# Optimization experiments

Hardware: AMD Instinct MI355X
Metric: run time of the kernel (lower is better)

## Reference

```python
import jax, jax.numpy as jnp
import numpy as np

TOP_K = 2
EPS = 1e-6


def setup_inputs() -> dict:
    key = jax.random.key(0)
    ks = jax.random.split(key, 4)
    T, H, D, E = 8192, 2048, 2048, 8
    std = 0.02
    return {
        "x": jax.random.normal(ks[0], (T, H), dtype=jnp.float32),
        "router_scale": jnp.ones((H,), dtype=jnp.float32),
        "per_expert_scale": jnp.ones((E,), dtype=jnp.float32),
        "router_w": jax.random.normal(ks[1], (E, H), dtype=jnp.float32) * std,
        "gate_up_proj": jax.random.normal(ks[2], (E, 2 * D, H), dtype=jnp.float32) * std,
        "down_proj": jax.random.normal(ks[3], (E, H, D), dtype=jnp.float32) * std,
    }


def reference(x, router_scale, per_expert_scale, router_w, gate_up_proj, down_proj):
    T, H = x.shape
    E = router_w.shape[0]
    D = down_proj.shape[-1]

    # RMSNorm (no learned scale) + router scaling
    r = x * jax.lax.rsqrt(jnp.mean(x * x, axis=-1, keepdims=True) + EPS)
    r = r * router_scale * (H ** -0.5)

    logits = (r @ router_w.T).astype(jnp.float32)          # [T, E]
    probs = jax.nn.softmax(logits, axis=-1)
    _, topk_idx = jax.lax.top_k(logits, TOP_K)             # [T, k]
    w = jnp.take_along_axis(probs, topk_idx, axis=-1)      # [T, k]
    w = w / jnp.sum(w, axis=-1, keepdims=True)
    w = w * per_expert_scale[topk_idx]

    # Dense combine weights [T, E]; zero for non-selected experts (topk indices
    # are distinct per token, so .set is collision-free).
    combine = jnp.zeros((T, E), dtype=x.dtype)
    combine = combine.at[jnp.arange(T)[:, None], topk_idx].set(w.astype(x.dtype))

    out = jnp.zeros_like(x)
    for e in range(E):  # fixed small loop over experts (structural, not data dim)
        gu = x @ gate_up_proj[e].T                          # [T, 2D]
        gate, up = gu[:, :D], gu[:, D:]
        h = jax.nn.gelu(gate, approximate=True) * up        # GLU with tanh-gelu
        out = out + combine[:, e:e + 1] * (h @ down_proj[e].T)
    return out
```

## Files before the change

kernel.cpp:

```cpp
#include <hip/hip_runtime.h>
#include <hip/hip_bf16.h>
#include <math.h>

#define TT 8192
#define HH 2048
#define DD 2048
#define EE 8
#define NT 32

typedef short bf16x8 __attribute__((ext_vector_type(8)));
typedef float f32x4 __attribute__((ext_vector_type(4)));

__device__ __forceinline__ ushort f2bf(float f){
  unsigned u = __float_as_uint(f);
  u += 0x7fffu + ((u>>16)&1u);
  return (ushort)(u>>16);
}

#define GLOAD16(SRC,DST) \
  __builtin_amdgcn_global_load_lds((const __attribute__((address_space(1))) void*)(SRC), \
                                   (__attribute__((address_space(3))) void*)(DST), 16, 0, 0)

#define SBAR __builtin_amdgcn_sched_barrier(0)
#define BARR __builtin_amdgcn_s_barrier()
#define WLG  asm volatile("s_waitcnt lgkmcnt(0)" ::: "memory")
#define WVM6 asm volatile("s_waitcnt vmcnt(6)" ::: "memory")
#define PRI(x) __builtin_amdgcn_s_setprio(x)

__global__ __launch_bounds__(256) void cvt_kernel(const float* __restrict__ src,
                                                  ushort* __restrict__ dst, size_t n){
  size_t i = ((size_t)blockIdx.x*256 + threadIdx.x)*8;
  size_t stride = (size_t)gridDim.x*256*8;
  for (; i < n; i += stride){
    float4 a = *(const float4*)(src+i);
    float4 b = *(const float4*)(src+i+4);
    uint4 v;
    v.x = (unsigned)f2bf(a.x) | ((unsigned)f2bf(a.y)<<16);
    v.y = (unsigned)f2bf(a.z) | ((unsigned)f2bf(a.w)<<16);
    v.z = (unsigned)f2bf(b.x) | ((unsigned)f2bf(b.y)<<16);
    v.w = (unsigned)f2bf(b.z) | ((unsigned)f2bf(b.w)<<16);
    *(uint4*)(dst+i) = v;
  }
}

__global__ __launch_bounds__(256) void router_kernel(
    const float* __restrict__ x, const float* __restrict__ rscale,
    const float* __restrict__ pes, const float* __restrict__ rw,
    ushort* __restrict__ x16, int* __restrict__ cnt,
    int* __restrict__ tok, float* __restrict__ wgt, int4* __restrict__ tmap)
{
  int t = blockIdx.x;
  int tid = threadIdx.x;
  const float4* xr  = (const float4*)(x + (size_t)t*HH);
  const float4* rs4 = (const float4*)rscale;
  float4 xa = xr[tid], xb = xr[tid+256];
  float4 sa = rs4[tid], sb = rs4[tid+256];
  double xd[8] = {xa.x,xa.y,xa.z,xa.w,xb.x,xb.y,xb.z,xb.w};
  double sd[8] = {sa.x,sa.y,sa.z,sa.w,sb.x,sb.y,sb.z,sb.w};
  double acc[9];
  double ss = 0.0;
  #pragma unroll
  for (int j=0;j<8;j++) ss += xd[j]*xd[j];
  acc[8] = ss;
  double xs[8];
  #pragma unroll
  for (int j=0;j<8;j++) xs[j] = xd[j]*sd[j];
  #pragma unroll
  for (int e=0;e<EE;e++){
    const float4* w4 = (const float4*)(rw + (size_t)e*HH);
    float4 wa = w4[tid], wb = w4[tid+256];
    double wd[8] = {wa.x,wa.y,wa.z,wa.w,wb.x,wb.y,wb.z,wb.w};
    double d = 0.0;
    #pragma unroll
    for (int j=0;j<8;j++) d += xs[j]*wd[j];
    acc[e] = d;
  }
  uint2 pa, pb;
  pa.x = (unsigned)f2bf(xa.x) | ((unsigned)f2bf(xa.y)<<16);
  pa.y = (unsigned)f2bf(xa.z) | ((unsigned)f2bf(xa.w)<<16);
  pb.x = (unsigned)f2bf(xb.x) | ((unsigned)f2bf(xb.y)<<16);
  pb.y = (unsigned)f2bf(xb.z) | ((unsigned)f2bf(xb.w)<<16);
  uint2* xo = (uint2*)(x16 + (size_t)t*HH);
  xo[tid] = pa; xo[tid+256] = pb;

  __shared__ double red[9*256];
  #pragma unroll
  for (int j=0;j<9;j++) red[j*256+tid] = acc[j];
  __syncthreads();
  for (int s=128;s>0;s>>=1){
    if (tid < s){
      #pragma unroll
      for (int j=0;j<9;j++) red[j*256+tid] += red[j*256+tid+s];
    }
    __syncthreads();
  }
  if (tid==0){
    double mean = red[8*256] / (double)HH;
    double rms  = 1.0 / sqrt(mean + 1e-6);
    double sc   = rms / sqrt((double)HH);
    double l[EE];
    #pragma unroll
    for (int e=0;e<EE;e++) l[e] = red[e*256]*sc;
    int i0 = 0;
    #pragma unroll
    for (int e=1;e<EE;e++) if (l[e] > l[i0]) i0 = e;
    int i1 = -1;
    #pragma unroll
    for (int e=0;e<EE;e++){ if (e==i0) continue; if (i1 < 0 || l[e] > l[i1]) i1 = e; }
    double p1 = exp(l[i1]-l[i0]);
    double s  = 1.0 + p1;
    float w0 = (float)((1.0/s) * (double)pes[i0]);
    float w1 = (float)((p1 /s) * (double)pes[i1]);
    int pos0 = atomicAdd(&cnt[i0],1);
    tok[i0*TT+pos0] = t; wgt[i0*TT+pos0] = w0;
    int pos1 = atomicAdd(&cnt[i1],1);
    tok[i1*TT+pos1] = t; wgt[i1*TT+pos1] = w1;
    tmap[t] = make_int4(i0,pos0,i1,pos1);
  }
}

__global__ void scan_kernel(const int* __restrict__ cnt, int* __restrict__ off){
  if (threadIdx.x==0 && blockIdx.x==0){
    int a = 0;
    for (int e=0;e<EE;e++){ off[e]=a; a+=cnt[e]; }
    off[EE]=a;
  }
}

#define STA(bb,h,t) do{ \
    GLOAD16(pA[2*(h)  ] + (size_t)(t)*64, &ldsA[bb][(h)*8192        + wid*512]); \
    GLOAD16(pA[2*(h)+1] + (size_t)(t)*64, &ldsA[bb][(h)*8192 + 4096 + wid*512]); }while(0)
#define STB(bb,h,t) do{ \
    GLOAD16(pB[2*(h)  ] + (size_t)(t)*64, &ldsB[bb][(h)*8192        + wid*512]); \
    GLOAD16(pB[2*(h)+1] + (size_t)(t)*64, &ldsB[bb][(h)*8192 + 4096 + wid*512]); }while(0)

#define RD_A(h) do{ _Pragma("unroll") \
  for (int mf=0;mf<4;mf++){ int row=(h)*128 + wm*64 + mf*16 + frow; \
    a[mf][0] = *(const bf16x8*)&As[row*64 + c0]; \
    a[mf][1] = *(const bf16x8*)&As[row*64 + c1]; } }while(0)
#define RD_B(h,bb_) do{ _Pragma("unroll") \
  for (int nf=0;nf<2;nf++){ int row=(h)*128 + wn*32 + nf*16 + frow; \
    bb_[nf][0] = *(const bf16x8*)&Bs[row*64 + c0]; \
    bb_[nf][1] = *(const bf16x8*)&Bs[row*64 + c1]; } }while(0)

#define MMQ(mo,no,bb_) do{ _Pragma("unroll") \
  for (int mf=0;mf<4;mf++){ _Pragma("unroll") \
    for (int nf=0;nf<2;nf++){ \
      acc[(mo)+mf][(no)+nf] = __builtin_amdgcn_mfma_f32_16x16x32_bf16(a[mf][0], bb_[nf][0], acc[(mo)+mf][(no)+nf],0,0,0); \
      acc[(mo)+mf][(no)+nf] = __builtin_amdgcn_mfma_f32_16x16x32_bf16(a[mf][1], bb_[nf][1], acc[(mo)+mf][(no)+nf],0,0,0); } } }while(0)

#define KLOOP for (int t=0;t<NT;t++){ \
    int cur=t&1, nxt=cur^1; \
    const ushort* As=&ldsA[cur][0]; const ushort* Bs=&ldsB[cur][0]; \
    RD_A(0); RD_B(0,b0); \
    if (t+1<NT) STA(nxt,1,t+1); \
    SBAR; BARR; WLG; SBAR; PRI(1); MMQ(0,0,b0); PRI(0); SBAR; BARR; SBAR; \
    RD_B(1,b1); \
    if (t+2<NT) STA(cur,0,t+2); \
    SBAR; BARR; WLG; SBAR; PRI(1); MMQ(0,2,b1); PRI(0); SBAR; BARR; SBAR; \
    RD_A(1); \
    if (t+2<NT) STB(cur,0,t+2); \
    SBAR; BARR; WLG; SBAR; PRI(1); MMQ(4,0,b0); PRI(0); SBAR; BARR; SBAR; \
    if (t+2<NT) STB(cur,1,t+2); \
    SBAR; BARR; SBAR; PRI(1); MMQ(4,2,b1); PRI(0); SBAR; WVM6; BARR; SBAR; \
  }

#define PROLOGUE \
  STA(0,0,0); STB(0,0,0); STB(0,1,0); STA(0,1,0); \
  STA(1,0,1); STB(1,0,1); STB(1,1,1); \
  SBAR; WVM6; BARR; SBAR;

__global__ __launch_bounds__(512,2) void ffn1_kernel(
    const ushort* __restrict__ x16, const ushort* __restrict__ w13,
    const int* __restrict__ cnt, const int* __restrict__ off,
    const int* __restrict__ tok, ushort* __restrict__ hbuf)
{
  int f = blockIdx.x + 16*(blockIdx.y + 32*blockIdx.z);
  int w = ((f&7)<<9) + (f>>3);
  int e  = w >> 9;
  int n0 = (w & 15) << 7;
  int m0 = ((w >> 4) & 31) << 8;
  int ce = cnt[e];
  if (m0 >= ce) return;

  __shared__ ushort ldsA[2][256*64];
  __shared__ ushort ldsB[2][256*64];

  int tid = threadIdx.x, wid = tid>>6, lane = tid&63;
  int wm = wid>>2, wn = wid&3;
  int frow = lane&15, klane = lane>>4;
  int c0 = ((klane  ) ^ (frow&7))<<3;
  int c1 = ((klane+4) ^ (frow&7))<<3;

  int r   = wid*8 + (lane>>3);
  int csw = ((lane&7) ^ (lane>>3))<<3;

  const ushort* pA[4]; const ushort* pB[4];
  int oe = off[e];
  #pragma unroll
  for (int k=0;k<4;k++){
    int R  = k*64 + r;
    int ar = min(m0+R, ce-1);
    pA[k] = x16 + (size_t)tok[e*TT+ar]*HH + csw;
    int p = 2*k + (r>>5), mat = (r>>4)&1;
    pB[k] = w13 + (size_t)e*(2*DD)*HH + (size_t)(mat*DD + n0 + p*16 + (r&15))*HH + csw;
  }

  f32x4 acc[8][4];
  #pragma unroll
  for (int i=0;i<8;i++)
    #pragma unroll
    for (int j=0;j<4;j++) acc[i][j] = {0.f,0.f,0.f,0.f};
  bf16x8 a[4][2], b0[2][2], b1[2][2];

  PROLOGUE
  KLOOP

  #pragma unroll
  for (int mf=0;mf<8;mf++){
    int rb = ((mf<4)? wm*64 + mf*16 : 128 + wm*64 + (mf-4)*16) + klane*4;
    #pragma unroll
    for (int q=0;q<4;q++){
      int gm = m0 + rb + q;
      if (gm < ce){
        size_t hrow = (size_t)(oe+gm)*DD;
        #pragma unroll
        for (int pp=0;pp<2;pp++){
          float g = acc[mf][2*pp][q], u = acc[mf][2*pp+1][q];
          float t2 = 1.5957691216057308f*(g + 0.044715f*g*g*g);
          float sg = 1.f/(1.f+__expf(-t2));
          hbuf[hrow + n0 + pp*64 + wn*16 + frow] = f2bf(g*u*sg);
        }
      }
    }
  }
}

__global__ __launch_bounds__(512,2) void ffn2_kernel(
    const ushort* __restrict__ hbuf, const ushort* __restrict__ w2,
    const int* __restrict__ cnt, const int* __restrict__ off,
    ushort* __restrict__ ybuf)
{
  int f = blockIdx.x + 8*(blockIdx.y + 32*blockIdx.z);
  int w = ((f&7)<<8) + (f>>3);
  int e  = w >> 8;
  int n0 = (w & 7) << 8;
  int m0 = ((w >> 3) & 31) << 8;
  int ce = cnt[e];
  if (m0 >= ce) return;

  __shared__ ushort ldsA[2][256*64];
  __shared__ ushort ldsB[2][256*64];

  int tid = threadIdx.x, wid = tid>>6, lane = tid&63;
  int wm = wid>>2, wn = wid&3;
  int frow = lane&15, klane = lane>>4;
  int c0 = ((klane  ) ^ (frow&7))<<3;
  int c1 = ((klane+4) ^ (frow&7))<<3;

  int r   = wid*8 + (lane>>3);
  int csw = ((lane&7) ^ (lane>>3))<<3;

  const ushort* pA[4]; const ushort* pB[4];
  int oe = off[e];
  #pragma unroll
  for (int k=0;k<4;k++){
    int R  = k*64 + r;
    int ar = oe + min(m0+R, ce-1);
    pA[k] = hbuf + (size_t)ar*DD + csw;
    pB[k] = w2 + (size_t)e*HH*DD + (size_t)(n0 + R)*DD + csw;
  }

  f32x4 acc[8][4];
  #pragma unroll
  for (int i=0;i<8;i++)
    #pragma unroll
    for (int j=0;j<4;j++) acc[i][j] = {0.f,0.f,0.f,0.f};
  bf16x8 a[4][2], b0[2][2], b1[2][2];

  PROLOGUE
  KLOOP

  #pragma unroll
  for (int mf=0;mf<8;mf++){
    int rb = ((mf<4)? wm*64 + mf*16 : 128 + wm*64 + (mf-4)*16) + klane*4;
    #pragma unroll
    for (int q=0;q<4;q++){
      int gm = m0 + rb + q;
      if (gm < ce){
        size_t yrow = (size_t)(oe+gm)*HH;
        #pragma unroll
        for (int nf=0;nf<4;nf++){
          int col = (nf>>1)*128 + wn*32 + (nf&1)*16 + frow;
          ybuf[yrow + n0 + col] = f2bf(acc[mf][nf][q]);
        }
      }
    }
  }
}

__global__ __launch_bounds__(256) void combine_kernel(
    const ushort* __restrict__ ybuf, const int4* __restrict__ tmap,
    const float* __restrict__ wgt, const int* __restrict__ off,
    float* __restrict__ out)
{
  int t = blockIdx.x, tid = threadIdx.x;
  int4 m = tmap[t];
  float w0 = wgt[m.x*TT + m.y];
  float w1 = wgt[m.z*TT + m.w];
  const ushort* y0 = ybuf + (size_t)(off[m.x] + m.y)*HH + tid*8;
  const ushort* y1 = ybuf + (size_t)(off[m.z] + m.w)*HH + tid*8;
  uint4 v0 = *(const uint4*)y0;
  uint4 v1 = *(const uint4*)y1;
  float* o = out + (size_t)t*HH + tid*8;
  const unsigned* a0 = (const unsigned*)&v0;
  const unsigned* a1 = (const unsigned*)&v1;
  float r[8];
  #pragma unroll
  for (int j=0;j<4;j++){
    float lo0 = __uint_as_float(a0[j]<<16), hi0 = __uint_as_float(a0[j]&0xffff0000u);
    float lo1 = __uint_as_float(a1[j]<<16), hi1 = __uint_as_float(a1[j]&0xffff0000u);
    r[2*j]   = w0*lo0 + w1*lo1;
    r[2*j+1] = w0*hi0 + w1*hi1;
  }
  *(float4*)o     = make_float4(r[0],r[1],r[2],r[3]);
  *(float4*)(o+4) = make_float4(r[4],r[5],r[6],r[7]);
}

extern "C" void kernel_launch(void* const* d_in, const int* in_sizes, int n_in,
                              void* d_out, int out_size, void* d_ws, size_t ws_size,
                              hipStream_t stream)
{
  const float* x    = (const float*)d_in[0];
  const float* rsc  = (const float*)d_in[1];
  const float* pes  = (const float*)d_in[2];
  const float* rw   = (const float*)d_in[3];
  const float* w13f = (const float*)d_in[4];
  const float* w2f  = (const float*)d_in[5];
  float* out = (float*)d_out;

  char* ws = (char*)d_ws;
  size_t o_x16 = 0;
  size_t o_w13 = o_x16 + (size_t)TT*HH*2;
  size_t o_w2  = o_w13 + (size_t)EE*2*DD*HH*2;
  size_t o_h   = o_w2  + (size_t)EE*HH*DD*2;
  size_t o_cnt = o_h   + (size_t)2*TT*DD*2;
  size_t o_off = o_cnt + 128;
  size_t o_tok = o_off + 128;
  size_t o_wgt = o_tok + (size_t)EE*TT*4;
  size_t o_map = o_wgt + (size_t)EE*TT*4;
  size_t need  = o_map + (size_t)TT*16;

  if (ws_size < need){ hipMemsetAsync(d_out, 0, (size_t)TT*HH*4, stream); return; }

  ushort* x16 = (ushort*)(ws + o_x16);
  ushort* w13 = (ushort*)(ws + o_w13);
  ushort* w2  = (ushort*)(ws + o_w2);
  ushort* hbuf= (ushort*)(ws + o_h);
  ushort* ybuf= (ushort*)(ws + o_w13);
  int*   cnt  = (int*)(ws + o_cnt);
  int*   off  = (int*)(ws + o_off);
  int*   tok  = (int*)(ws + o_tok);
  float* wgt  = (float*)(ws + o_wgt);
  int4*  tmap = (int4*)(ws + o_map);

  hipMemsetAsync(cnt, 0, EE*sizeof(int), stream);
  cvt_kernel<<<4096,256,0,stream>>>(w13f, w13, (size_t)EE*2*DD*HH);
  cvt_kernel<<<2048,256,0,stream>>>(w2f,  w2,  (size_t)EE*HH*DD);
  router_kernel<<<TT,256,0,stream>>>(x, rsc, pes, rw, x16, cnt, tok, wgt, tmap);
  scan_kernel<<<1,64,0,stream>>>(cnt, off);
  dim3 g1(DD/128, TT/256, EE);
  ffn1_kernel<<<g1,512,0,stream>>>(x16, w13, cnt, off, tok, hbuf);
  dim3 g2(HH/256, TT/256, EE);
  ffn2_kernel<<<g2,512,0,stream>>>(hbuf, w2, cnt, off, ybuf);
  combine_kernel<<<TT,256,0,stream>>>(ybuf, tmap, wgt, off, out);
}
```

Measured before the change: 791.3 us.

## Fuse fp32-to-bf16 weight conversion into expert GEMM B-tile loads

Removes the separate weight conversion kernels and has both FFN GEMMs load fp32 weights into registers, convert them to bf16 and store them into swizzled LDS. The k-loop pipeline is reordered so the register load for step t+2 and the LDS write for step t+1 overlap with MFMA work. This removes a full pass over all expert weights. In exchange, the weights are read in fp32 by every active m-tile, and register pressure rises.

```diff
diff --git a/kernel.cpp b/kernel.cpp
--- a/kernel.cpp
+++ b/kernel.cpp
@@ -24,24 +24,7 @@
 #define SBAR __builtin_amdgcn_sched_barrier(0)
 #define BARR __builtin_amdgcn_s_barrier()
 #define WLG  asm volatile("s_waitcnt lgkmcnt(0)" ::: "memory")
-#define WVM6 asm volatile("s_waitcnt vmcnt(6)" ::: "memory")
 #define PRI(x) __builtin_amdgcn_s_setprio(x)
-
-__global__ __launch_bounds__(256) void cvt_kernel(const float* __restrict__ src,
-                                                  ushort* __restrict__ dst, size_t n){
-  size_t i = ((size_t)blockIdx.x*256 + threadIdx.x)*8;
-  size_t stride = (size_t)gridDim.x*256*8;
-  for (; i < n; i += stride){
-    float4 a = *(const float4*)(src+i);
-    float4 b = *(const float4*)(src+i+4);
-    uint4 v;
-    v.x = (unsigned)f2bf(a.x) | ((unsigned)f2bf(a.y)<<16);
-    v.y = (unsigned)f2bf(a.z) | ((unsigned)f2bf(a.w)<<16);
-    v.z = (unsigned)f2bf(b.x) | ((unsigned)f2bf(b.y)<<16);
-    v.w = (unsigned)f2bf(b.z) | ((unsigned)f2bf(b.w)<<16);
-    *(uint4*)(dst+i) = v;
-  }
-}
 
 __global__ __launch_bounds__(256) void router_kernel(
     const float* __restrict__ x, const float* __restrict__ rscale,
@@ -130,9 +113,17 @@
 #define STA(bb,h,t) do{ \
     GLOAD16(pA[2*(h)  ] + (size_t)(t)*64, &ldsA[bb][(h)*8192        + wid*512]); \
     GLOAD16(pA[2*(h)+1] + (size_t)(t)*64, &ldsA[bb][(h)*8192 + 4096 + wid*512]); }while(0)
-#define STB(bb,h,t) do{ \
-    GLOAD16(pB[2*(h)  ] + (size_t)(t)*64, &ldsB[bb][(h)*8192        + wid*512]); \
-    GLOAD16(pB[2*(h)+1] + (size_t)(t)*64, &ldsB[bb][(h)*8192 + 4096 + wid*512]); }while(0)
+
+#define BLOAD(t) do{ _Pragma("unroll") \
+  for (int j=0;j<8;j++) breg[j] = *(const float4*)(pBsrc + (size_t)(t)*64 + j*4); }while(0)
+#define BWRITE(bb) do{ _Pragma("unroll") \
+  for (int j=0;j<4;j++){ \
+    uint4 v; \
+    v.x=(unsigned)f2bf(breg[2*j  ].x)|((unsigned)f2bf(breg[2*j  ].y)<<16); \
+    v.y=(unsigned)f2bf(breg[2*j  ].z)|((unsigned)f2bf(breg[2*j  ].w)<<16); \
+    v.z=(unsigned)f2bf(breg[2*j+1].x)|((unsigned)f2bf(breg[2*j+1].y)<<16); \
+    v.w=(unsigned)f2bf(breg[2*j+1].z)|((unsigned)f2bf(breg[2*j+1].w)<<16); \
+    *(uint4*)&ldsB[bb][(bwr<<6) + (((bch*4+j) ^ (bwr&7))<<3)] = v; } }while(0)
 
 #define RD_A(h) do{ _Pragma("unroll") \
   for (int mf=0;mf<4;mf++){ int row=(h)*128 + wm*64 + mf*16 + frow; \
@@ -153,25 +144,27 @@
     int cur=t&1, nxt=cur^1; \
     const ushort* As=&ldsA[cur][0]; const ushort* Bs=&ldsB[cur][0]; \
     RD_A(0); RD_B(0,b0); \
-    if (t+1<NT) STA(nxt,1,t+1); \
     SBAR; BARR; WLG; SBAR; PRI(1); MMQ(0,0,b0); PRI(0); SBAR; BARR; SBAR; \
     RD_B(1,b1); \
     if (t+2<NT) STA(cur,0,t+2); \
     SBAR; BARR; WLG; SBAR; PRI(1); MMQ(0,2,b1); PRI(0); SBAR; BARR; SBAR; \
     RD_A(1); \
-    if (t+2<NT) STB(cur,0,t+2); \
+    if (t+1<NT) BWRITE(nxt); \
     SBAR; BARR; WLG; SBAR; PRI(1); MMQ(4,0,b0); PRI(0); SBAR; BARR; SBAR; \
-    if (t+2<NT) STB(cur,1,t+2); \
-    SBAR; BARR; SBAR; PRI(1); MMQ(4,2,b1); PRI(0); SBAR; WVM6; BARR; SBAR; \
+    if (t+2<NT){ STA(cur,1,t+2); BLOAD(t+2); } \
+    SBAR; BARR; SBAR; PRI(1); MMQ(4,2,b1); PRI(0); SBAR; BARR; SBAR; \
   }
 
 #define PROLOGUE \
-  STA(0,0,0); STB(0,0,0); STB(0,1,0); STA(0,1,0); \
-  STA(1,0,1); STB(1,0,1); STB(1,1,1); \
-  SBAR; WVM6; BARR; SBAR;
+  BLOAD(0); \
+  STA(0,0,0); STA(0,1,0); STA(1,0,1); STA(1,1,1); \
+  BWRITE(0); \
+  BLOAD(1); \
+  asm volatile("s_waitcnt vmcnt(12)" ::: "memory"); \
+  WLG; BARR; SBAR;
 
 __global__ __launch_bounds__(512,2) void ffn1_kernel(
-    const ushort* __restrict__ x16, const ushort* __restrict__ w13,
+    const ushort* __restrict__ x16, const float* __restrict__ w13,
     const int* __restrict__ cnt, const int* __restrict__ off,
     const int* __restrict__ tok, ushort* __restrict__ hbuf)
 {
@@ -195,16 +188,18 @@
   int r   = wid*8 + (lane>>3);
   int csw = ((lane&7) ^ (lane>>3))<<3;
 
-  const ushort* pA[4]; const ushort* pB[4];
+  const ushort* pA[4];
   int oe = off[e];
   #pragma unroll
   for (int k=0;k<4;k++){
     int R  = k*64 + r;
     int ar = min(m0+R, ce-1);
     pA[k] = x16 + (size_t)tok[e*TT+ar]*HH + csw;
-    int p = 2*k + (r>>5), mat = (r>>4)&1;
-    pB[k] = w13 + (size_t)e*(2*DD)*HH + (size_t)(mat*DD + n0 + p*16 + (r&15))*HH + csw;
-  }
+  }
+  int bwr = tid & 255, bch = tid >> 8;
+  const float* pBsrc = w13 + (size_t)e*(2*DD)*HH
+                     + (size_t)(((bwr>>4)&1)*DD + n0 + (bwr>>5)*16 + (bwr&15))*HH
+                     + bch*32;
 
   f32x4 acc[8][4];
   #pragma unroll
@@ -212,6 +207,7 @@
     #pragma unroll
     for (int j=0;j<4;j++) acc[i][j] = {0.f,0.f,0.f,0.f};
   bf16x8 a[4][2], b0[2][2], b1[2][2];
+  float4 breg[8];
 
   PROLOGUE
   KLOOP
@@ -237,7 +233,7 @@
 }
 
 __global__ __launch_bounds__(512,2) void ffn2_kernel(
-    const ushort* __restrict__ hbuf, const ushort* __restrict__ w2,
+    const ushort* __restrict__ hbuf, const float* __restrict__ w2,
     const int* __restrict__ cnt, const int* __restrict__ off,
     ushort* __restrict__ ybuf)
 {
@@ -261,15 +257,16 @@
   int r   = wid*8 + (lane>>3);
   int csw = ((lane&7) ^ (lane>>3))<<3;
 
-  const ushort* pA[4]; const ushort* pB[4];
+  const ushort* pA[4];
   int oe = off[e];
   #pragma unroll
   for (int k=0;k<4;k++){
     int R  = k*64 + r;
     int ar = oe + min(m0+R, ce-1);
     pA[k] = hbuf + (size_t)ar*DD + csw;
-    pB[k] = w2 + (size_t)e*HH*DD + (size_t)(n0 + R)*DD + csw;
-  }
+  }
+  int bwr = tid & 255, bch = tid >> 8;
+  const float* pBsrc = w2 + (size_t)e*HH*DD + (size_t)(n0 + bwr)*DD + bch*32;
 
   f32x4 acc[8][4];
   #pragma unroll
@@ -277,6 +274,7 @@
     #pragma unroll
     for (int j=0;j<4;j++) acc[i][j] = {0.f,0.f,0.f,0.f};
   bf16x8 a[4][2], b0[2][2], b1[2][2];
+  float4 breg[8];
 
   PROLOGUE
   KLOOP
@@ -341,10 +339,9 @@
 
   char* ws = (char*)d_ws;
   size_t o_x16 = 0;
-  size_t o_w13 = o_x16 + (size_t)TT*HH*2;
-  size_t o_w2  = o_w13 + (size_t)EE*2*DD*HH*2;
-  size_t o_h   = o_w2  + (size_t)EE*HH*DD*2;
-  size_t o_cnt = o_h   + (size_t)2*TT*DD*2;
+  size_t o_h   = o_x16 + (size_t)TT*HH*2;
+  size_t o_y   = o_h   + (size_t)2*TT*DD*2;
+  size_t o_cnt = o_y   + (size_t)2*TT*HH*2;
   size_t o_off = o_cnt + 128;
   size_t o_tok = o_off + 128;
   size_t o_wgt = o_tok + (size_t)EE*TT*4;
@@ -354,10 +351,8 @@
   if (ws_size < need){ hipMemsetAsync(d_out, 0, (size_t)TT*HH*4, stream); return; }
 
   ushort* x16 = (ushort*)(ws + o_x16);
-  ushort* w13 = (ushort*)(ws + o_w13);
-  ushort* w2  = (ushort*)(ws + o_w2);
   ushort* hbuf= (ushort*)(ws + o_h);
-  ushort* ybuf= (ushort*)(ws + o_w13);
+  ushort* ybuf= (ushort*)(ws + o_y);
   int*   cnt  = (int*)(ws + o_cnt);
   int*   off  = (int*)(ws + o_off);
   int*   tok  = (int*)(ws + o_tok);
@@ -365,13 +360,11 @@
   int4*  tmap = (int4*)(ws + o_map);
 
   hipMemsetAsync(cnt, 0, EE*sizeof(int), stream);
-  cvt_kernel<<<4096,256,0,stream>>>(w13f, w13, (size_t)EE*2*DD*HH);
-  cvt_kernel<<<2048,256,0,stream>>>(w2f,  w2,  (size_t)EE*HH*DD);
   router_kernel<<<TT,256,0,stream>>>(x, rsc, pes, rw, x16, cnt, tok, wgt, tmap);
   scan_kernel<<<1,64,0,stream>>>(cnt, off);
   dim3 g1(DD/128, TT/256, EE);
-  ffn1_kernel<<<g1,512,0,stream>>>(x16, w13, cnt, off, tok, hbuf);
+  ffn1_kernel<<<g1,512,0,stream>>>(x16, w13f, cnt, off, tok, hbuf);
   dim3 g2(HH/256, TT/256, EE);
-  ffn2_kernel<<<g2,512,0,stream>>>(hbuf, w2, cnt, off, ybuf);
+  ffn2_kernel<<<g2,512,0,stream>>>(hbuf, w2f, cnt, off, ybuf);
   combine_kernel<<<TT,256,0,stream>>>(ybuf, tmap, wgt, off, out);
 }
```

Result: slower. 1.377 ms (+74.0%).

## Fuse weight bf16 conversions into router and ffn1 kernels

Applied to the files above, without the earlier changes.

Removes the two standalone fp32-to-bf16 conversion kernels. The gate_up weight conversion now runs as a grid-stride tail of the router kernel, and the down_proj conversion runs as a tail of the ffn1 kernel, including in blocks that have no tokens and previously exited early. This saves two launches and lets the bandwidth-bound conversion overlap with router and GEMM work. In exchange it adds memory traffic inside the ffn1 GEMM, which may slow it, and it relies on the ffn1 grid size being hard-coded to 4096 blocks.

```diff
diff --git a/kernel.cpp b/kernel.cpp
--- a/kernel.cpp
+++ b/kernel.cpp
@@ -27,27 +27,22 @@
 #define WVM6 asm volatile("s_waitcnt vmcnt(6)" ::: "memory")
 #define PRI(x) __builtin_amdgcn_s_setprio(x)
 
-__global__ __launch_bounds__(256) void cvt_kernel(const float* __restrict__ src,
-                                                  ushort* __restrict__ dst, size_t n){
-  size_t i = ((size_t)blockIdx.x*256 + threadIdx.x)*8;
-  size_t stride = (size_t)gridDim.x*256*8;
-  for (; i < n; i += stride){
-    float4 a = *(const float4*)(src+i);
-    float4 b = *(const float4*)(src+i+4);
-    uint4 v;
-    v.x = (unsigned)f2bf(a.x) | ((unsigned)f2bf(a.y)<<16);
-    v.y = (unsigned)f2bf(a.z) | ((unsigned)f2bf(a.w)<<16);
-    v.z = (unsigned)f2bf(b.x) | ((unsigned)f2bf(b.y)<<16);
-    v.w = (unsigned)f2bf(b.z) | ((unsigned)f2bf(b.w)<<16);
-    *(uint4*)(dst+i) = v;
-  }
-}
+#define CVT8(SRCP,DSTP,CI) do{ \
+    const float* _s = (SRCP) + (CI)*8; \
+    float4 _a = *(const float4*)_s, _b = *(const float4*)(_s+4); \
+    uint4 _v; \
+    _v.x=(unsigned)f2bf(_a.x)|((unsigned)f2bf(_a.y)<<16); \
+    _v.y=(unsigned)f2bf(_a.z)|((unsigned)f2bf(_a.w)<<16); \
+    _v.z=(unsigned)f2bf(_b.x)|((unsigned)f2bf(_b.y)<<16); \
+    _v.w=(unsigned)f2bf(_b.z)|((unsigned)f2bf(_b.w)<<16); \
+    *(uint4*)((DSTP) + (CI)*8) = _v; }while(0)
 
 __global__ __launch_bounds__(256) void router_kernel(
     const float* __restrict__ x, const float* __restrict__ rscale,
     const float* __restrict__ pes, const float* __restrict__ rw,
     ushort* __restrict__ x16, int* __restrict__ cnt,
-    int* __restrict__ tok, float* __restrict__ wgt, int4* __restrict__ tmap)
+    int* __restrict__ tok, float* __restrict__ wgt, int4* __restrict__ tmap,
+    const float* __restrict__ w13f, ushort* __restrict__ w13b)
 {
   int t = blockIdx.x;
   int tid = threadIdx.x;
@@ -116,6 +111,13 @@
     int pos1 = atomicAdd(&cnt[i1],1);
     tok[i1*TT+pos1] = t; wgt[i1*TT+pos1] = w1;
     tmap[t] = make_int4(i0,pos0,i1,pos1);
+  }
+
+  {
+    size_t gid    = (size_t)t*256 + tid;
+    size_t nchunk = (size_t)EE*2*DD*HH/8;
+    size_t stride = (size_t)TT*256;
+    for (size_t c = gid; c < nchunk; c += stride) CVT8(w13f, w13b, c);
   }
 }
 
@@ -173,7 +175,8 @@
 __global__ __launch_bounds__(512,2) void ffn1_kernel(
     const ushort* __restrict__ x16, const ushort* __restrict__ w13,
     const int* __restrict__ cnt, const int* __restrict__ off,
-    const int* __restrict__ tok, ushort* __restrict__ hbuf)
+    const int* __restrict__ tok, ushort* __restrict__ hbuf,
+    const float* __restrict__ w2f, ushort* __restrict__ w2b)
 {
   int f = blockIdx.x + 16*(blockIdx.y + 32*blockIdx.z);
   int w = ((f&7)<<9) + (f>>3);
@@ -181,58 +184,67 @@
   int n0 = (w & 15) << 7;
   int m0 = ((w >> 4) & 31) << 8;
   int ce = cnt[e];
-  if (m0 >= ce) return;
 
   __shared__ ushort ldsA[2][256*64];
   __shared__ ushort ldsB[2][256*64];
 
   int tid = threadIdx.x, wid = tid>>6, lane = tid&63;
-  int wm = wid>>2, wn = wid&3;
-  int frow = lane&15, klane = lane>>4;
-  int c0 = ((klane  ) ^ (frow&7))<<3;
-  int c1 = ((klane+4) ^ (frow&7))<<3;
-
-  int r   = wid*8 + (lane>>3);
-  int csw = ((lane&7) ^ (lane>>3))<<3;
-
-  const ushort* pA[4]; const ushort* pB[4];
-  int oe = off[e];
-  #pragma unroll
-  for (int k=0;k<4;k++){
-    int R  = k*64 + r;
-    int ar = min(m0+R, ce-1);
-    pA[k] = x16 + (size_t)tok[e*TT+ar]*HH + csw;
-    int p = 2*k + (r>>5), mat = (r>>4)&1;
-    pB[k] = w13 + (size_t)e*(2*DD)*HH + (size_t)(mat*DD + n0 + p*16 + (r&15))*HH + csw;
-  }
-
-  f32x4 acc[8][4];
-  #pragma unroll
-  for (int i=0;i<8;i++)
-    #pragma unroll
-    for (int j=0;j<4;j++) acc[i][j] = {0.f,0.f,0.f,0.f};
-  bf16x8 a[4][2], b0[2][2], b1[2][2];
-
-  PROLOGUE
-  KLOOP
-
-  #pragma unroll
-  for (int mf=0;mf<8;mf++){
-    int rb = ((mf<4)? wm*64 + mf*16 : 128 + wm*64 + (mf-4)*16) + klane*4;
-    #pragma unroll
-    for (int q=0;q<4;q++){
-      int gm = m0 + rb + q;
-      if (gm < ce){
-        size_t hrow = (size_t)(oe+gm)*DD;
-        #pragma unroll
-        for (int pp=0;pp<2;pp++){
-          float g = acc[mf][2*pp][q], u = acc[mf][2*pp+1][q];
-          float t2 = 1.5957691216057308f*(g + 0.044715f*g*g*g);
-          float sg = 1.f/(1.f+__expf(-t2));
-          hbuf[hrow + n0 + pp*64 + wn*16 + frow] = f2bf(g*u*sg);
+
+  if (m0 < ce){
+    int wm = wid>>2, wn = wid&3;
+    int frow = lane&15, klane = lane>>4;
+    int c0 = ((klane  ) ^ (frow&7))<<3;
+    int c1 = ((klane+4) ^ (frow&7))<<3;
+
+    int r   = wid*8 + (lane>>3);
+    int csw = ((lane&7) ^ (lane>>3))<<3;
+
+    const ushort* pA[4]; const ushort* pB[4];
+    int oe = off[e];
+    #pragma unroll
+    for (int k=0;k<4;k++){
+      int R  = k*64 + r;
+      int ar = min(m0+R, ce-1);
+      pA[k] = x16 + (size_t)tok[e*TT+ar]*HH + csw;
+      int p = 2*k + (r>>5), mat = (r>>4)&1;
+      pB[k] = w13 + (size_t)e*(2*DD)*HH + (size_t)(mat*DD + n0 + p*16 + (r&15))*HH + csw;
+    }
+
+    f32x4 acc[8][4];
+    #pragma unroll
+    for (int i=0;i<8;i++)
+      #pragma unroll
+      for (int j=0;j<4;j++) acc[i][j] = {0.f,0.f,0.f,0.f};
+    bf16x8 a[4][2], b0[2][2], b1[2][2];
+
+    PROLOGUE
+    KLOOP
+
+    #pragma unroll
+    for (int mf=0;mf<8;mf++){
+      int rb = ((mf<4)? wm*64 + mf*16 : 128 + wm*64 + (mf-4)*16) + klane*4;
+      #pragma unroll
+      for (int q=0;q<4;q++){
+        int gm = m0 + rb + q;
+        if (gm < ce){
+          size_t hrow = (size_t)(oe+gm)*DD;
+          #pragma unroll
+          for (int pp=0;pp<2;pp++){
+            float g = acc[mf][2*pp][q], u = acc[mf][2*pp+1][q];
+            float t2 = 1.5957691216057308f*(g + 0.044715f*g*g*g);
+            float sg = 1.f/(1.f+__expf(-t2));
+            hbuf[hrow + n0 + pp*64 + wn*16 + frow] = f2bf(g*u*sg);
+          }
         }
       }
     }
+  }
+
+  {
+    size_t gid    = (size_t)f*512 + tid;
+    size_t nchunk = (size_t)EE*HH*DD/8;
+    size_t stride = (size_t)4096*512;
+    for (size_t c = gid; c < nchunk; c += stride) CVT8(w2f, w2b, c);
   }
 }
 
@@ -354,8 +366,8 @@
   if (ws_size < need){ hipMemsetAsync(d_out, 0, (size_t)TT*HH*4, stream); return; }
 
   ushort* x16 = (ushort*)(ws + o_x16);
-  ushort* w13 = (ushort*)(ws + o_w13);
-  ushort* w2  = (ushort*)(ws + o_w2);
+  ushort* w13b= (ushort*)(ws + o_w13);
+  ushort* w2b = (ushort*)(ws + o_w2);
   ushort* hbuf= (ushort*)(ws + o_h);
   ushort* ybuf= (ushort*)(ws + o_w13);
   int*   cnt  = (int*)(ws + o_cnt);
@@ -365,13 +377,11 @@
   int4*  tmap = (int4*)(ws + o_map);
 
   hipMemsetAsync(cnt, 0, EE*sizeof(int), stream);
-  cvt_kernel<<<4096,256,0,stream>>>(w13f, w13, (size_t)EE*2*DD*HH);
-  cvt_kernel<<<2048,256,0,stream>>>(w2f,  w2,  (size_t)EE*HH*DD);
-  router_kernel<<<TT,256,0,stream>>>(x, rsc, pes, rw, x16, cnt, tok, wgt, tmap);
+  router_kernel<<<TT,256,0,stream>>>(x, rsc, pes, rw, x16, cnt, tok, wgt, tmap, w13f, w13b);
   scan_kernel<<<1,64,0,stream>>>(cnt, off);
   dim3 g1(DD/128, TT/256, EE);
-  ffn1_kernel<<<g1,512,0,stream>>>(x16, w13, cnt, off, tok, hbuf);
+  ffn1_kernel<<<g1,512,0,stream>>>(x16, w13b, cnt, off, tok, hbuf, w2f, w2b);
   dim3 g2(HH/256, TT/256, EE);
-  ffn2_kernel<<<g2,512,0,stream>>>(hbuf, w2, cnt, off, ybuf);
+  ffn2_kernel<<<g2,512,0,stream>>>(hbuf, w2b, cnt, off, ybuf);
   combine_kernel<<<TT,256,0,stream>>>(ybuf, tmap, wgt, off, out);
 }
```

New measurement: 711.8 us. 10.0% less time.
